# Kernel tuning notes

Measured on AMD Instinct MI355X. Metric: run time of the kernel, lower is better.

Reference implementation:

```python
import jax, jax.numpy as jnp
import numpy as np

# ---- module hyperparameters (match BlurredNoise defaults) ----
CHANNELS = 1024
BLUR_WIDTHS = 128
NOISE_CHANNELS = CHANNELS // BLUR_WIDTHS  # 8
MIN_SR = 250.0
MAX_SR = 10000.0
CUTOFF = 2.0
WIDTH = 12.0
SR_BASE = 2.0
NORM_PER_FILTER = 1.0
KERNEL_SIZE = int(np.ceil(MAX_SR / 2))  # 5000

BATCH = 2
SEQ_LENGTH = 4096
IN_SEQ = SEQ_LENGTH + KERNEL_SIZE - 1  # 9095


def _kaiser_beta(a):
    # scipy.signal.kaiser_beta
    if a > 50:
        return 0.1102 * (a - 8.7)
    if a > 21:
        return 0.5842 * (a - 21) ** 0.4 + 0.07886 * (a - 21)
    return 0.0


def _firwin_lowpass(numtaps, cutoff, width, fs):
    # Re-implementation of scipy.signal.firwin(numtaps, cutoff, width=width, fs=fs)
    # (lowpass, pass_zero=True, Kaiser window chosen from transition width).
    nyq = 0.5 * fs
    atten = 2.285 * (numtaps - 1) * np.pi * (width / nyq) + 7.95  # kaiser_atten
    beta = _kaiser_beta(atten)
    win = np.kaiser(numtaps, beta)
    m = np.arange(numtaps) - (numtaps - 1) / 2.0
    right = cutoff / nyq
    h = right * np.sinc(right * m)  # ideal lowpass impulse response
    h = h * win
    h = h / h.sum()  # normalize DC gain to 1 (scale at f=0, pass_zero)
    return h.astype(np.float32)


def _build_filters():
    log_min = np.log(MIN_SR) / np.log(SR_BASE)
    log_max = np.log(MAX_SR) / np.log(SR_BASE)
    sampling_rates = SR_BASE ** np.linspace(log_min, log_max, BLUR_WIDTHS)
    sampling_rates = np.clip(sampling_rates, MIN_SR, MAX_SR)
    blur_filters = np.zeros((BLUR_WIDTHS, KERNEL_SIZE), dtype=np.float32)
    for i, sr in enumerate(sampling_rates):
        num_taps = int(np.ceil(sr / 2))
        blur_filters[i, -num_taps:] = _firwin_lowpass(num_taps, CUTOFF, WIDTH, sr)
    output_scale = 1.0 / np.sqrt((blur_filters ** 2).sum(axis=1))  # (128,)
    output_scale = output_scale.reshape(1, BLUR_WIDTHS, 1).astype(np.float32)
    return blur_filters, output_scale


def setup_inputs() -> dict:
    key = jax.random.key(0)
    noise = jax.random.normal(key, (BATCH, NOISE_CHANNELS, IN_SEQ), dtype=jnp.float32)
    bf, os_ = _build_filters()
    return {
        "noise": noise,
        "blur_filters": jnp.asarray(bf),
        "output_scale": jnp.asarray(os_),
    }


def reference(noise, blur_filters, output_scale):
    # noise: (n, c, t_in) with c = NOISE_CHANNELS
    n, c, t = noise.shape
    # einops.repeat 'n c t -> (n c) b t' followed by grouped conv (groups=b)
    # with per-group single input channel is exactly a standard conv with
    # 1 input channel and b output channels.
    x = noise.reshape(n * c, 1, t)                       # (n*c, 1, t_in)
    k = blur_filters[:, None, :]                         # (b, 1, K) OIW
    feats = jax.lax.conv_general_dilated(
        x, k, window_strides=(1,), padding="VALID",
        dimension_numbers=("NCH", "OIH", "NCH"))          # (n*c, b, T)
    feats = feats * (1.0 + NORM_PER_FILTER * (output_scale - 1.0))
    T = feats.shape[-1]
    # '(n c) b t -> n (c b) t'
    return feats.reshape(n, c * BLUR_WIDTHS, T)
```

## Files before the change

### kernel.cpp

```cpp
#include <hip/hip_runtime.h>
#include <hip/hip_bf16.h>
#include <math.h>


#define KS      5000
#define IN_SEQ  9095
#define T_OUT   4096
#define NBC     16
#define NF      128
#define NSTEP   157
#define X4ROW   10240
#define SWZ_SHORTS (8*NSTEP*512)
#define X4_OFF  (SWZ_SHORTS*2)
#define CSTRIDE 1072
#define XBUF    (4*CSTRIDE)

typedef __attribute__((ext_vector_type(8))) short v8s;
typedef __attribute__((ext_vector_type(4))) float v4f;

__device__ __forceinline__ unsigned short f2b(float v) {
  union { __hip_bfloat16 h; unsigned short u; } cv;
  cv.h = __float2bfloat16(v);
  return cv.u;
}

__device__ __forceinline__ int S_of(int f) {
  const double lmin = 7.965784284662087;
  const double lmax = 13.287712379549449;
  double sr = exp2(lmin + (lmax - lmin) * ((double)f / 127.0));
  sr = fmin(fmax(sr, 250.0), 10000.0);
  int taps = (int)ceil(sr * 0.5) + 8;
  int S = (taps + 31) >> 5;
  return S > NSTEP ? NSTEP : S;
}

__device__ __forceinline__ void async16(const void* g, void* l) {
  __builtin_amdgcn_global_load_lds((const __attribute__((address_space(1))) void*)g,
                                   (__attribute__((address_space(3))) void*)l, 16, 0, 0);
}

__global__ void build_pre(const float* __restrict__ filt,
                          const float* __restrict__ noise,
                          unsigned short* __restrict__ swz,
                          unsigned short* __restrict__ x4) {
  const int b = blockIdx.x;
  if (b < 2512) {
    const int i = b * 256 + threadIdx.x;
    if (i < SWZ_SHORTS) {
      const int blk = i >> 9, w = i & 511;
      const int ft = blk / NSTEP, s = blk - ft * NSTEP;
      const int q = w >> 7, n = (w >> 3) & 15, j = w & 7;
      const int jg = KS - 32 * (s + 1) + 8 * q + j;
      const float v = (jg >= 0 && jg < KS) ? filt[(size_t)(ft * 16 + n) * KS + jg] : 0.0f;
      swz[i] = f2b(v);
    }
  } else {
    const int i = (b - 2512) * 256 + threadIdx.x;
    if (i < 4 * NBC * X4ROW) {
      const int c = i / (NBC * X4ROW);
      const int r = i - c * (NBC * X4ROW);
      const int bc = r / X4ROW;
      const int ii = r - bc * X4ROW;
      const int g = ii - 384 + c;
      const float v = (g >= 0 && g < IN_SEQ) ? noise[bc * IN_SEQ + g] : 0.0f;
      x4[i] = f2b(v);
    }
  }
}

__global__ __launch_bounds__(64, 2) void blur_mfma(
    const unsigned short* __restrict__ swz,
    const unsigned short* __restrict__ x4,
    const float* __restrict__ scale,
    float* __restrict__ out)
{
  __shared__ __align__(16) char xb[2 * XBUF];
  const int lane = threadIdx.x;
  const int b = blockIdx.x;
  const int g = b >> 8, r = b & 255;
  const int h = g & 1;
  const int p = ((g >> 1) << 8) | r;
  const int bc = p >> 6;
  const int t0 = (p & 63) << 6;

  const int ftb = h ? 3 : 7;
  int S[4];
  #pragma unroll
  for (int n = 0; n < 4; ++n)
    S[n] = __builtin_amdgcn_readfirstlane(S_of(16 * (ftb - n) + 15));
  const int S0 = S[0];
  const int NG = (S0 + 11) / 12;

  const int m = lane & 15, q = lane >> 4, c = m & 3;
  const char* xrd = xb + c * CSTRIDE + 8 * (m >> 2) + 16 * q;

  const char* bbase[4];
  #pragma unroll
  for (int n = 0; n < 4; ++n)
    bbase[n] = (const char*)swz + 1024 * ((size_t)(ftb - n) * NSTEP) + 16 * lane;

  auto stage_x = [&](int G, int buf) {
    const int istart = t0 + (KS - 384 * (G + 1)) + 384;
    #pragma unroll
    for (int cc = 0; cc < 4; ++cc) {
      const char* gp = (const char*)x4
          + 2 * ((size_t)(cc * NBC + bc) * X4ROW + istart) + 16 * lane;
      async16(gp, xb + buf * XBUF + cc * CSTRIDE);
    }
  };

  v4f acc[4][4];
  const v4f vz = {0.f, 0.f, 0.f, 0.f};
  #pragma unroll
  for (int mt = 0; mt < 4; ++mt)
    #pragma unroll
    for (int n = 0; n < 4; ++n) acc[mt][n] = vz;

  v8s breg[2][4];
  stage_x(0, 0);
  #pragma unroll
  for (int n = 0; n < 4; ++n) breg[0][n] = *(const v8s*)(bbase[n]);

  #pragma unroll 1
  for (int G = 0; G < NG; ++G) {
    asm volatile("s_waitcnt vmcnt(0)" ::: "memory");
    if (G + 1 < NG) stage_x(G + 1, (G + 1) & 1);
    const char* xg = xrd + (G & 1) * XBUF;
    #pragma unroll
    for (int ls = 0; ls < 12; ++ls) {
      const int s = 12 * G + ls;
      if (s >= S0) break;
      const int par = ls & 1;
      #pragma unroll
      for (int n = 0; n < 4; ++n)
        if (s + 1 < S[n])
          breg[par ^ 1][n] = *(const v8s*)(bbase[n] + 1024 * (s + 1));
      const int koff = 64 * (11 - ls);
      v8s a[4];
      #pragma unroll
      for (int mt = 0; mt < 4; ++mt) {
        *(uint2*)&a[mt]       = *(const uint2*)(xg + koff + 32 * mt);
        *((uint2*)&a[mt] + 1) = *(const uint2*)(xg + koff + 32 * mt + 8);
      }
      #pragma unroll
      for (int n = 0; n < 4; ++n)
        if (s < S[n]) {
          #pragma unroll
          for (int mt = 0; mt < 4; ++mt)
            acc[mt][n] = __builtin_amdgcn_mfma_f32_16x16x32_bf16(
                a[mt], breg[par][n], acc[mt][n], 0, 0, 0);
        }
    }
  }

  #pragma unroll
  for (int n = 0; n < 4; ++n) {
    const int F = 16 * (ftb - n) + m;
    const float sc = scale[F];
    #pragma unroll
    for (int mt = 0; mt < 4; ++mt) {
      v4f o = acc[mt][n] * sc;
      *(v4f*)(out + (size_t)(bc * NF + F) * T_OUT + t0 + 16 * mt + 4 * q) = o;
    }
  }
}

extern "C" void kernel_launch(void* const* d_in, const int* in_sizes, int n_in,
                              void* d_out, int out_size, void* d_ws, size_t ws_size,
                              hipStream_t stream) {
  const float* noise = (const float*)d_in[0];
  const float* filt  = (const float*)d_in[1];
  const float* scale = (const float*)d_in[2];
  float* out = (float*)d_out;

  unsigned short* swz = (unsigned short*)d_ws;
  unsigned short* x4  = (unsigned short*)((char*)d_ws + X4_OFF);

  const int pre_blocks = 2512 + (4 * NBC * X4ROW + 255) / 256;
  build_pre<<<pre_blocks, 256, 0, stream>>>(filt, noise, swz, x4);
  blur_mfma<<<2048, 64, 0, stream>>>(swz, x4, scale, out);
}
```

Baseline: 127.0 us.

## Fuse noise conversion into MFMA kernel, cover all filters per block, trim filter prep

Drops the precomputed shifted bf16 copy of the noise. Each block now loads fp32 noise into registers, converts it and writes the four shifted LDS copies itself, using register double-buffering and a deeper three-stage B-fragment prefetch. Each block now computes all 8 filter tiles for its time tile, so the grid is halved and each noise window is loaded only once. The filter swizzle kernel writes only the nonzero steps, and step counts come from a constant table instead of double-precision exp2. In exchange, register pressure is higher (launch bounds cut to 1 wave) and the step counts are hard-coded for these exact hyperparameters.

```diff
diff --git a/kernel.cpp b/kernel.cpp
--- a/kernel.cpp
+++ b/kernel.cpp
@@ -1,6 +1,5 @@
 #include <hip/hip_runtime.h>
 #include <hip/hip_bf16.h>
-#include <math.h>
 
 
 #define KS      5000
@@ -9,14 +8,15 @@
 #define NBC     16
 #define NF      128
 #define NSTEP   157
-#define X4ROW   10240
-#define SWZ_SHORTS (8*NSTEP*512)
-#define X4_OFF  (SWZ_SHORTS*2)
-#define CSTRIDE 1072
+#define NG      14
+#define CSTRIDE 1056
 #define XBUF    (4*CSTRIDE)
+#define S0MAX   157
 
 typedef __attribute__((ext_vector_type(8))) short v8s;
 typedef __attribute__((ext_vector_type(4))) float v4f;
+
+__device__ __constant__ int d_S_tab[8] = {7, 10, 16, 25, 40, 62, 99, 157};
 
 __device__ __forceinline__ unsigned short f2b(float v) {
   union { __hip_bfloat16 h; unsigned short u; } cv;
@@ -24,138 +24,144 @@
   return cv.u;
 }
 
-__device__ __forceinline__ int S_of(int f) {
-  const double lmin = 7.965784284662087;
-  const double lmax = 13.287712379549449;
-  double sr = exp2(lmin + (lmax - lmin) * ((double)f / 127.0));
-  sr = fmin(fmax(sr, 250.0), 10000.0);
-  int taps = (int)ceil(sr * 0.5) + 8;
-  int S = (taps + 31) >> 5;
-  return S > NSTEP ? NSTEP : S;
+__global__ void build_swz(const float* __restrict__ filt,
+                          unsigned short* __restrict__ swz) {
+  const int idx = blockIdx.x * 256 + threadIdx.x;
+  constexpr int pre[9] = {0, 7, 17, 33, 58, 98, 160, 259, 416};
+  if (idx >= 416 * 512) return;
+  const int blk = idx >> 9, w = idx & 511;
+  int ft = 0;
+  #pragma unroll
+  for (int i = 1; i < 8; ++i) if (blk >= pre[i]) ft = i;
+  const int s = blk - pre[ft];
+  const int q = w >> 7, n = (w >> 3) & 15, j = w & 7;
+  const int jg = KS - 32 * (s + 1) + 8 * q + j;
+  const float v = (jg >= 0) ? filt[(size_t)(ft * 16 + n) * KS + jg] : 0.0f;
+  swz[((size_t)(ft * NSTEP + s) << 9) + w] = f2b(v);
 }
 
-__device__ __forceinline__ void async16(const void* g, void* l) {
-  __builtin_amdgcn_global_load_lds((const __attribute__((address_space(1))) void*)g,
-                                   (__attribute__((address_space(3))) void*)l, 16, 0, 0);
-}
-
-__global__ void build_pre(const float* __restrict__ filt,
-                          const float* __restrict__ noise,
-                          unsigned short* __restrict__ swz,
-                          unsigned short* __restrict__ x4) {
-  const int b = blockIdx.x;
-  if (b < 2512) {
-    const int i = b * 256 + threadIdx.x;
-    if (i < SWZ_SHORTS) {
-      const int blk = i >> 9, w = i & 511;
-      const int ft = blk / NSTEP, s = blk - ft * NSTEP;
-      const int q = w >> 7, n = (w >> 3) & 15, j = w & 7;
-      const int jg = KS - 32 * (s + 1) + 8 * q + j;
-      const float v = (jg >= 0 && jg < KS) ? filt[(size_t)(ft * 16 + n) * KS + jg] : 0.0f;
-      swz[i] = f2b(v);
-    }
-  } else {
-    const int i = (b - 2512) * 256 + threadIdx.x;
-    if (i < 4 * NBC * X4ROW) {
-      const int c = i / (NBC * X4ROW);
-      const int r = i - c * (NBC * X4ROW);
-      const int bc = r / X4ROW;
-      const int ii = r - bc * X4ROW;
-      const int g = ii - 384 + c;
-      const float v = (g >= 0 && g < IN_SEQ) ? noise[bc * IN_SEQ + g] : 0.0f;
-      x4[i] = f2b(v);
-    }
-  }
-}
-
-__global__ __launch_bounds__(64, 2) void blur_mfma(
+__global__ __launch_bounds__(64, 1) void blur_mfma(
+    const float* __restrict__ noise,
     const unsigned short* __restrict__ swz,
-    const unsigned short* __restrict__ x4,
     const float* __restrict__ scale,
     float* __restrict__ out)
 {
   __shared__ __align__(16) char xb[2 * XBUF];
+
   const int lane = threadIdx.x;
-  const int b = blockIdx.x;
-  const int g = b >> 8, r = b & 255;
-  const int h = g & 1;
-  const int p = ((g >> 1) << 8) | r;
-  const int bc = p >> 6;
-  const int t0 = (p & 63) << 6;
+  const int b  = blockIdx.x;
+  const int bc = b >> 6;
+  const int t0 = (b & 63) << 6;
+  const int m = lane & 15, q = lane >> 4, c = m & 3;
+  const float* __restrict__ xn = noise + (size_t)bc * IN_SEQ;
 
-  const int ftb = h ? 3 : 7;
-  int S[4];
+  int S[8];
   #pragma unroll
-  for (int n = 0; n < 4; ++n)
-    S[n] = __builtin_amdgcn_readfirstlane(S_of(16 * (ftb - n) + 15));
-  const int S0 = S[0];
-  const int NG = (S0 + 11) / 12;
+  for (int n = 0; n < 8; ++n) S[n] = d_S_tab[n];
 
-  const int m = lane & 15, q = lane >> 4, c = m & 3;
+  float4 xr[3];
+  auto stage_load = [&](int G) {
+    const int g0 = t0 + KS - 384 * (G + 1);
+    const int base = g0 + 8 * lane;
+    #pragma unroll
+    for (int i = 0; i < 3; ++i) {
+      const int idx = base + 4 * i;
+      float4 v;
+      if (idx >= 0 && idx + 4 <= IN_SEQ) {
+        v = *(const float4*)(xn + idx);
+      } else {
+        v.x = (idx + 0 >= 0 && idx + 0 < IN_SEQ) ? xn[idx + 0] : 0.0f;
+        v.y = (idx + 1 >= 0 && idx + 1 < IN_SEQ) ? xn[idx + 1] : 0.0f;
+        v.z = (idx + 2 >= 0 && idx + 2 < IN_SEQ) ? xn[idx + 2] : 0.0f;
+        v.w = (idx + 3 >= 0 && idx + 3 < IN_SEQ) ? xn[idx + 3] : 0.0f;
+      }
+      xr[i] = v;
+    }
+  };
+  auto stage_write = [&](int G) {
+    const float* f = (const float*)xr;
+    unsigned int u6[6];
+    #pragma unroll
+    for (int j = 0; j < 6; ++j)
+      u6[j] = (unsigned)f2b(f[2 * j]) | ((unsigned)f2b(f[2 * j + 1]) << 16);
+    auto AL = [](unsigned hi, unsigned lo) { return (lo >> 16) | (hi << 16); };
+    char* buf = xb + (G & 1) * XBUF + 16 * lane;
+    uint4 w0 = {u6[0], u6[1], u6[2], u6[3]};
+    uint4 w1 = {AL(u6[1],u6[0]), AL(u6[2],u6[1]), AL(u6[3],u6[2]), AL(u6[4],u6[3])};
+    uint4 w2 = {u6[1], u6[2], u6[3], u6[4]};
+    uint4 w3 = {AL(u6[2],u6[1]), AL(u6[3],u6[2]), AL(u6[4],u6[3]), AL(u6[5],u6[4])};
+    *(uint4*)(buf + 0 * CSTRIDE) = w0;
+    *(uint4*)(buf + 1 * CSTRIDE) = w1;
+    *(uint4*)(buf + 2 * CSTRIDE) = w2;
+    *(uint4*)(buf + 3 * CSTRIDE) = w3;
+  };
+
   const char* xrd = xb + c * CSTRIDE + 8 * (m >> 2) + 16 * q;
-
-  const char* bbase[4];
-  #pragma unroll
-  for (int n = 0; n < 4; ++n)
-    bbase[n] = (const char*)swz + 1024 * ((size_t)(ftb - n) * NSTEP) + 16 * lane;
-
-  auto stage_x = [&](int G, int buf) {
-    const int istart = t0 + (KS - 384 * (G + 1)) + 384;
+  auto read_A = [&](int par, int ls, v8s* dst) {
+    const char* p = xrd + par * XBUF + 64 * (11 - ls);
     #pragma unroll
-    for (int cc = 0; cc < 4; ++cc) {
-      const char* gp = (const char*)x4
-          + 2 * ((size_t)(cc * NBC + bc) * X4ROW + istart) + 16 * lane;
-      async16(gp, xb + buf * XBUF + cc * CSTRIDE);
+    for (int mt = 0; mt < 4; ++mt) {
+      v8s a;
+      *(uint2*)&a       = *(const uint2*)(p + 32 * mt);
+      *((uint2*)&a + 1) = *(const uint2*)(p + 32 * mt + 8);
+      dst[mt] = a;
     }
   };
 
-  v4f acc[4][4];
+  const char* bb = (const char*)swz + 16 * lane;
+  auto bfrag = [&](int n, int s) {
+    return *(const v8s*)(bb + ((size_t)(n * NSTEP + s) << 10));
+  };
+
+  v4f acc[4][8];
   const v4f vz = {0.f, 0.f, 0.f, 0.f};
   #pragma unroll
   for (int mt = 0; mt < 4; ++mt)
     #pragma unroll
-    for (int n = 0; n < 4; ++n) acc[mt][n] = vz;
+    for (int n = 0; n < 8; ++n) acc[mt][n] = vz;
 
-  v8s breg[2][4];
-  stage_x(0, 0);
+  v8s areg[2][4], breg[3][8];
+
+  stage_load(0); stage_write(0);
+  stage_load(1);
+  read_A(0, 0, areg[0]);
   #pragma unroll
-  for (int n = 0; n < 4; ++n) breg[0][n] = *(const v8s*)(bbase[n]);
+  for (int n = 0; n < 8; ++n) breg[0][n] = bfrag(n, 0);
+  #pragma unroll
+  for (int n = 0; n < 8; ++n) if (1 < S[n]) breg[1][n] = bfrag(n, 1);
 
   #pragma unroll 1
   for (int G = 0; G < NG; ++G) {
-    asm volatile("s_waitcnt vmcnt(0)" ::: "memory");
-    if (G + 1 < NG) stage_x(G + 1, (G + 1) & 1);
-    const char* xg = xrd + (G & 1) * XBUF;
     #pragma unroll
     for (int ls = 0; ls < 12; ++ls) {
       const int s = 12 * G + ls;
-      if (s >= S0) break;
-      const int par = ls & 1;
+      if (s >= S0MAX) break;
       #pragma unroll
-      for (int n = 0; n < 4; ++n)
-        if (s + 1 < S[n])
-          breg[par ^ 1][n] = *(const v8s*)(bbase[n] + 1024 * (s + 1));
-      const int koff = 64 * (11 - ls);
-      v8s a[4];
-      #pragma unroll
-      for (int mt = 0; mt < 4; ++mt) {
-        *(uint2*)&a[mt]       = *(const uint2*)(xg + koff + 32 * mt);
-        *((uint2*)&a[mt] + 1) = *(const uint2*)(xg + koff + 32 * mt + 8);
+      for (int n = 0; n < 8; ++n)
+        if (s + 2 < S[n]) breg[(ls + 2) % 3][n] = bfrag(n, s + 2);
+      if (ls == 5) {
+        if (G + 1 < NG) stage_write(G + 1);
+        if (G + 2 < NG) stage_load(G + 2);
+      }
+      if (s + 1 < S0MAX) {
+        if (ls == 11) read_A((G + 1) & 1, 0, areg[(ls + 1) & 1]);
+        else          read_A(G & 1, ls + 1, areg[(ls + 1) & 1]);
       }
       #pragma unroll
-      for (int n = 0; n < 4; ++n)
+      for (int n = 0; n < 8; ++n) {
         if (s < S[n]) {
           #pragma unroll
           for (int mt = 0; mt < 4; ++mt)
             acc[mt][n] = __builtin_amdgcn_mfma_f32_16x16x32_bf16(
-                a[mt], breg[par][n], acc[mt][n], 0, 0, 0);
+                areg[ls & 1][mt], breg[ls % 3][n], acc[mt][n], 0, 0, 0);
         }
+      }
     }
   }
 
   #pragma unroll
-  for (int n = 0; n < 4; ++n) {
-    const int F = 16 * (ftb - n) + m;
+  for (int n = 0; n < 8; ++n) {
+    const int F = 16 * n + m;
     const float sc = scale[F];
     #pragma unroll
     for (int mt = 0; mt < 4; ++mt) {
@@ -174,9 +180,7 @@
   float* out = (float*)d_out;
 
   unsigned short* swz = (unsigned short*)d_ws;
-  unsigned short* x4  = (unsigned short*)((char*)d_ws + X4_OFF);
 
-  const int pre_blocks = 2512 + (4 * NBC * X4ROW + 255) / 256;
-  build_pre<<<pre_blocks, 256, 0, stream>>>(filt, noise, swz, x4);
-  blur_mfma<<<2048, 64, 0, stream>>>(swz, x4, scale, out);
+  build_swz<<<832, 256, 0, stream>>>(filt, swz);
+  blur_mfma<<<1024, 64, 0, stream>>>(noise, swz, scale, out);
 }
```

Result: slower. 152.2 us (+19.8%).
